# Optimization experiments

Hardware: AMD Instinct MI355X
Metric: run time of the kernel (lower is better)

Reference implementation:

```python
import jax, jax.numpy as jnp
import numpy as np

NUM_HEADS = 8
EPS = 1e-5  # torch GroupNorm default eps


def setup_inputs() -> dict:
    key = jax.random.key(0)
    ks = jax.random.split(key, 3)
    B, C, H, W = 8, 384, 32, 32
    x = jax.random.normal(ks[0], (B, C, H, W), dtype=jnp.float32)
    qkv_w = jax.random.normal(ks[1], (3 * C, C), dtype=jnp.float32) * 0.02
    proj_w = jax.random.normal(ks[2], (C, C), dtype=jnp.float32) * 0.02
    proj_b = jnp.zeros((C,), dtype=jnp.float32)
    lambda_param = jnp.ones((1, NUM_HEADS, 1, 1), dtype=jnp.float32) * 0.5
    gc = NUM_HEADS * ((C // NUM_HEADS) // 2)  # 192 group-norm channels
    gn_weight = jnp.ones((gc,), dtype=jnp.float32)
    gn_bias = jnp.zeros((gc,), dtype=jnp.float32)
    return {"x": x, "qkv_w": qkv_w, "lambda_param": lambda_param,
            "gn_weight": gn_weight, "gn_bias": gn_bias,
            "proj_w": proj_w, "proj_b": proj_b}


def reference(x, qkv_w, lambda_param, gn_weight, gn_bias, proj_w, proj_b):
    B, C, H, W = x.shape
    nh = NUM_HEADS
    hd = C // nh
    hd2 = hd // 2
    N = H * W
    scale = hd ** -0.5

    xf = x.reshape(B, C, N)
    qkv = jnp.einsum('oc,bcn->bon', qkv_w, xf)  # (B, 3C, N), 1x1 conv no bias
    q, k, v = jnp.split(qkv, 3, axis=1)
    q = q.reshape(B, nh, hd, N)
    k = k.reshape(B, nh, hd, N)
    v = v.reshape(B, nh, hd, N)

    q1, q2 = q[:, :, :hd2], q[:, :, hd2:]
    k1, k2 = k[:, :, :hd2], k[:, :, hd2:]
    v1, v2 = v[:, :, :hd2], v[:, :, hd2:]

    # GroupNorm(2 groups) on q2 viewed as (B, nh*hd2, H, W)
    gc = nh * hd2
    qg = q2.reshape(B, 2, (gc // 2) * N)  # normalize over (group channels, H, W)
    mean = qg.mean(axis=2, keepdims=True)
    var = qg.var(axis=2, keepdims=True)
    qg = (qg - mean) * jax.lax.rsqrt(var + EPS)
    q2n = qg.reshape(B, gc, N) * gn_weight[None, :, None] + gn_bias[None, :, None]
    q2n = q2n.reshape(B, nh, hd2, N)

    # dual softmax attention maps (B, nh, N, N)
    attn1 = jax.nn.softmax(jnp.einsum('bhdn,bhdm->bhnm', q1, k1) * scale, axis=-1)
    attn2 = jax.nn.softmax(jnp.einsum('bhdn,bhdm->bhnm', q2n, k2) * scale * lambda_param, axis=-1)
    diff = attn1 - attn2

    out1 = jnp.einsum('bhnm,bhdm->bhnd', diff, v1)  # (B, nh, N, hd2)
    out2 = jnp.einsum('bhnm,bhdm->bhnd', diff, v2)
    out = jnp.concatenate([out1, out2], axis=2)  # (B, nh, 2N, hd2) -- matches torch cat dim=2
    out = out.reshape(B, C, H, W)

    out = jnp.einsum('oc,bchw->bohw', proj_w, out) + proj_b[None, :, None, None]
    return out
```

## Files before the change

### kernel.cpp

```cpp
#include <hip/hip_runtime.h>
#include <hip/hip_bf16.h>
#include <stdint.h>

typedef _Float16 half8 __attribute__((ext_vector_type(8)));
typedef _Float16 half4 __attribute__((ext_vector_type(4)));
typedef __fp16 fp16x2 __attribute__((ext_vector_type(2)));
typedef float floatx4 __attribute__((ext_vector_type(4)));
typedef float floatx16 __attribute__((ext_vector_type(16)));

#define SCALE 0.14433756729740643f
#define LOG2E 1.4426950408889634f


__device__ inline float fexp2(float x) { return __builtin_exp2f(x); }

__device__ inline uint32_t pkrtz(float a, float b) {
  fp16x2 h = __builtin_amdgcn_cvt_pkrtz(a, b);
  union { fp16x2 h; uint32_t u; } cv; cv.h = h; return cv.u;
}

__launch_bounds__(256)
__global__ void k_prep(const float* __restrict__ qkv_w, const float* __restrict__ pw,
                       const float* __restrict__ x, _Float16* __restrict__ Wf,
                       _Float16* __restrict__ PWf, _Float16* __restrict__ Xt) {
  const int bid = blockIdx.x;
  if (bid < 288) {
    const float* src = (bid < 216) ? qkv_w : pw;
    _Float16* dst = (bid < 216) ? Wf : PWf;
    int cid = (bid < 216 ? bid : bid - 216) * 256 + threadIdx.x;
    int nchunks = (bid < 216) ? 55296 : 18432;
    if (cid >= nchunks) return;
    int lane = cid & 63;
    int t = cid >> 6;
    int cb = t % 12;
    int g16 = t / 12;
    const float* s = src + (long)(g16 * 16 + (lane & 15)) * 384 + cb * 32 + (lane >> 4) * 8;
    floatx4 a = *(const floatx4*)s;
    floatx4 b = *(const floatx4*)(s + 4);
    half8 h;
    #pragma unroll
    for (int j = 0; j < 4; j++) { h[j] = (_Float16)a[j]; h[j+4] = (_Float16)b[j]; }
    *(half8*)(dst + (long)cid * 8) = h;
  } else {
    int idx = bid - 288;
    const int cblk = idx % 12, nseg = (idx / 12) & 3, b = idx / 48;
    const float* S = x + ((long)b * 384 + cblk * 32) * 1024 + nseg * 256;
    _Float16* D = Xt + (long)b * 393216 + cblk * 32768 + (long)nseg * 256 * 32;
    __shared__ _Float16 T[32][264];
    const int wv = threadIdx.x >> 6, lane = threadIdx.x & 63;
    #pragma unroll
    for (int rr = 0; rr < 8; rr++) {
      int r = wv * 8 + rr;
      floatx4 v = *(const floatx4*)(S + (long)r * 1024 + lane * 4);
      half4 h;
      #pragma unroll
      for (int j = 0; j < 4; j++) h[j] = (_Float16)v[j];
      *(half4*)&T[r][lane * 4] = h;
    }
    __syncthreads();
    const int nn = threadIdx.x >> 3, c = (threadIdx.x & 7) * 4;
    #pragma unroll
    for (int p = 0; p < 8; p++) {
      int n = p * 32 + nn;
      half4 h;
      #pragma unroll
      for (int i = 0; i < 4; i++) h[i] = T[c + i][n];
      *(half4*)(D + (long)n * 32 + c) = h;
    }
  }
}

__launch_bounds__(256)
__global__ void k_trh(const _Float16* __restrict__ src, _Float16* __restrict__ dst) {
  const int cblk = blockIdx.x, nseg = blockIdx.y, b = blockIdx.z;
  const _Float16* S = src + ((long)b * 384 + cblk * 32) * 1024 + nseg * 256;
  _Float16* D = dst + (long)b * 393216 + cblk * 32768 + (long)nseg * 256 * 32;
  __shared__ _Float16 T[32][264];
  const int wv = threadIdx.x >> 6, lane = threadIdx.x & 63;
  #pragma unroll
  for (int rr = 0; rr < 8; rr++) {
    int r = wv * 8 + rr;
    *(half4*)&T[r][lane * 4] = *(const half4*)(S + (long)r * 1024 + lane * 4);
  }
  __syncthreads();
  const int nn = threadIdx.x >> 3, c = (threadIdx.x & 7) * 4;
  #pragma unroll
  for (int p = 0; p < 8; p++) {
    int n = p * 32 + nn;
    half4 h;
    #pragma unroll
    for (int i = 0; i < 4; i++) h[i] = T[c + i][n];
    *(half4*)(D + (long)n * 32 + c) = h;
  }
}

__launch_bounds__(256, 4)
__global__ void k_qkv(const _Float16* __restrict__ Xt, const _Float16* __restrict__ Wf,
                      _Float16* __restrict__ Qs, _Float16* __restrict__ Ks,
                      _Float16* __restrict__ Vs, float* __restrict__ gnpart) {
  const int tid = threadIdx.x;
  const int lane = tid & 63;
  const int wv = tid >> 6;
  const int l15 = lane & 15;
  const int g = lane >> 4;
  const int o0 = blockIdx.x * 48;
  const int n0 = blockIdx.y * 64;
  const int b = blockIdx.z;

  const int ncol = n0 + wv * 16 + l15;
  const _Float16* xp = Xt + (long)b * 393216 + (long)ncol * 32 + g * 8;
  const _Float16* wfb = Wf + (long)(blockIdx.x * 36) * 512 + lane * 8;

  half8 xb[12];
  #pragma unroll
  for (int cb = 0; cb < 12; cb++) xb[cb] = *(const half8*)(xp + cb * 32768);

  floatx4 zero4 = {0.f, 0.f, 0.f, 0.f};
  floatx4 acc0 = zero4, acc1 = zero4, acc2 = zero4;

  half8 A0 = *(const half8*)(wfb);
  half8 A1 = *(const half8*)(wfb + 12 * 512);
  half8 A2 = *(const half8*)(wfb + 24 * 512);
  #pragma unroll
  for (int cb = 0; cb < 12; cb++) {
    half8 c0 = A0, c1 = A1, c2 = A2;
    if (cb < 11) {
      A0 = *(const half8*)(wfb + (cb + 1) * 512);
      A1 = *(const half8*)(wfb + (12 + cb + 1) * 512);
      A2 = *(const half8*)(wfb + (24 + cb + 1) * 512);
    }
    acc0 = __builtin_amdgcn_mfma_f32_16x16x32_f16(c0, xb[cb], acc0, 0, 0, 0);
    acc1 = __builtin_amdgcn_mfma_f32_16x16x32_f16(c1, xb[cb], acc1, 0, 0, 0);
    acc2 = __builtin_amdgcn_mfma_f32_16x16x32_f16(c2, xb[cb], acc2, 0, 0, 0);
  }

  floatx4 acc[3] = {acc0, acc1, acc2};
  __shared__ __align__(16) _Float16 T[3456];
  __shared__ float red[8];

  if (o0 < 768) {
    #pragma unroll
    for (int rt = 0; rt < 3; rt++)
      #pragma unroll
      for (int r = 0; r < 4; r++)
        T[(wv * 16 + l15) * 52 + rt * 16 + g * 4 + r] = (_Float16)acc[rt][r];
    __syncthreads();
    const int qk = o0 >= 384;
    const int hh = (o0 - qk * 384) / 48;
    _Float16* base = (qk ? Ks : Qs) + (long)(b * 8 + hh) * 65536;
    #pragma unroll
    for (int it = 0; it < 2; it++) {
      int slot = it * 256 + tid;
      int ntl = slot >> 8;
      int t   = (slot >> 6) & 3;
      int ln  = slot & 63;
      int hi_s = ln >> 5, l31_s = ln & 31;
      int n_ = ntl * 32 + l31_s;
      int c0 = t * 16 + hi_s * 8;
      half8 val;
      #pragma unroll
      for (int j = 0; j < 8; j++) {
        int col = c0 + j;
        int d48 = col < 24 ? col : col - 8;
        bool isq = (col < 24) || (col >= 32 && col < 56);
        val[j] = isq ? T[n_ * 52 + d48] : (_Float16)0;
      }
      *(half8*)(base + ((((n0 >> 5) + ntl) * 4 + t) * 64 + ln) * 8) = val;
    }
    if (!qk) {
      float s1 = 0.f, s2 = 0.f;
      int n_ = tid >> 2, k0 = (tid & 3) * 6;
      #pragma unroll
      for (int k = 0; k < 6; k++) {
        float v = (float)T[n_ * 52 + 24 + k0 + k];
        s1 += v; s2 += v * v;
      }
      #pragma unroll
      for (int off = 32; off > 0; off >>= 1) {
        s1 += __shfl_down(s1, off);
        s2 += __shfl_down(s2, off);
      }
      if ((tid & 63) == 0) { red[tid >> 6] = s1; red[4 + (tid >> 6)] = s2; }
      __syncthreads();
      if (tid == 0) {
        int slot = (b * 8 + hh) * 16 + (n0 >> 6);
        gnpart[slot * 2]     = red[0] + red[1] + red[2] + red[3];
        gnpart[slot * 2 + 1] = red[4] + red[5] + red[6] + red[7];
      }
    }
  } else {
    #pragma unroll
    for (int rt = 0; rt < 3; rt++)
      #pragma unroll
      for (int r = 0; r < 4; r++)
        T[(rt * 16 + g * 4 + r) * 72 + wv * 16 + l15] = (_Float16)acc[rt][r];
    __syncthreads();
    const int hh = (o0 - 768) / 48;
    _Float16* base = Vs + (long)(b * 8 + hh) * 65536;
    #pragma unroll
    for (int it = 0; it < 2; it++) {
      int slot = it * 256 + tid;
      int lwin = slot >> 8;
      int ckc  = (slot >> 6) & 3;
      int kc   = ckc & 1, c = ckc >> 1;
      int ln = slot & 63;
      int hi_s = ln >> 5, l31_s = ln & 31;
      int d48 = c * 32 + l31_s;
      half8 val;
      if (d48 < 48) {
        int mb = lwin * 32 + kc * 16 + hi_s * 4;
        half4 a = *(const half4*)&T[d48 * 72 + mb];
        half4 bq = *(const half4*)&T[d48 * 72 + mb + 8];
        val[0] = a[0]; val[1] = a[1]; val[2] = a[2]; val[3] = a[3];
        val[4] = bq[0]; val[5] = bq[1]; val[6] = bq[2]; val[7] = bq[3];
      } else {
        _Float16 f = (d48 == 48) ? (_Float16)1 : (_Float16)0;
        #pragma unroll
        for (int j = 0; j < 8; j++) val[j] = f;
      }
      *(half8*)(base + ((((n0 >> 5) + lwin) * 4 + ckc) * 64 + ln) * 8) = val;
    }
  }
}

__launch_bounds__(512, 4)
__global__ void k_attn(const _Float16* __restrict__ Qs, const _Float16* __restrict__ Ks,
                       const _Float16* __restrict__ Vs, const float* __restrict__ gnpart,
                       const float* __restrict__ lam, const float* __restrict__ gw,
                       const float* __restrict__ gb, _Float16* __restrict__ Yf) {
  const int tid = threadIdx.x;
  const int lane = tid & 63;
  const int wv = tid >> 6;
  const int l31 = lane & 31;
  const int hi = lane >> 5;
  const int id = blockIdx.x;
  const int bh = ((id >> 6) << 3) | (id & 7);
  const int ntlgrp = (id >> 3) & 7;
  const int br = wv & 1;
  const int ntile = ntlgrp * 4 + (wv >> 1);
  const int n0 = ntile * 32;
  const int b = bh >> 3, h = bh & 7;

  const _Float16* Qp = Qs + (long)bh * 65536 + (ntile * 256 + lane) * 8;
  half8 qra = *(const half8*)(Qp + (2 * br) * 512);
  half8 qrb = *(const half8*)(Qp + (2 * br + 1) * 512);
  half8 qfa, qfb;
  if (br == 0) {
    const float s1s = SCALE * LOG2E;
    #pragma unroll
    for (int j = 0; j < 8; j++) {
      qfa[j] = (_Float16)((float)qra[j] * s1s);
      qfb[j] = (_Float16)((float)qrb[j] * s1s);
    }
  } else {
    const int grp = h >> 2;
    const float* pp = gnpart + (b * 128 + grp * 64) * 2;
    float S1 = pp[lane * 2], S2 = pp[lane * 2 + 1];
    #pragma unroll
    for (int off = 1; off < 64; off <<= 1) {
      S1 += __shfl_xor(S1, off);
      S2 += __shfl_xor(S2, off);
    }
    float mean = S1 * (1.f / 98304.f);
    float rstd = rsqrtf(S2 * (1.f / 98304.f) - mean * mean + 1e-5f);
    float sl = SCALE * LOG2E * lam[h];
    const float* gwp = gw + h * 24;
    const float* gbp = gb + h * 24;
    #pragma unroll
    for (int j = 0; j < 8; j++) {
      qfa[j] = (_Float16)((((float)qra[j] - mean) * rstd * gwp[hi * 8 + j] + gbp[hi * 8 + j]) * sl);
      qfb[j] = (_Float16)((((float)qrb[j] - mean) * rstd * gwp[16 + j] + gbp[16 + j]) * sl);
    }
  }

  const _Float16* gK = Ks + (long)bh * 65536 + ((wv >> 2) * 2048 + (wv & 3) * 512) + lane * 8;
  const _Float16* gV = Vs + (long)bh * 65536 + ((wv >> 2) * 2048 + (wv & 3) * 512) + lane * 8;

  __shared__ __align__(16) char smem[32768];
  const int ldsK = wv * 1024 + lane * 16;
  const int ldsV = 8192 + wv * 1024 + lane * 16;

  floatx16 z16;
  #pragma unroll
  for (int i = 0; i < 16; i++) z16[i] = 0.f;
  floatx16 accA = z16, accB = z16;

  {
    uint4 a = *(const uint4*)gK;
    uint4 c = *(const uint4*)gV;
    *(uint4*)(smem + ldsK) = a;
    *(uint4*)(smem + ldsV) = c;
  }
  __syncthreads();

  #pragma unroll 2
  for (int i = 0; i < 16; i++) {
    const int cur = (i & 1) << 14;
    uint4 sa, sc;
    if (i < 15) {
      sa = *(const uint4*)(gK + (i + 1) * 4096);
      sc = *(const uint4*)(gV + (i + 1) * 4096);
    }
    #pragma unroll
    for (int j = 0; j < 2; j++) {
      const char* Kb = smem + cur + j * 4096;
      const char* Vb = smem + cur + 8192 + j * 4096;
      half8 kfa = *(const half8*)(Kb + (2 * br) * 1024 + lane * 16);
      half8 kfb = *(const half8*)(Kb + (2 * br + 1) * 1024 + lane * 16);

      floatx16 s = __builtin_amdgcn_mfma_f32_32x32x16_f16(kfa, qfa, z16, 0, 0, 0);
      s = __builtin_amdgcn_mfma_f32_32x32x16_f16(kfb, qfb, s, 0, 0, 0);

      half8 vf0 = *(const half8*)(Vb + lane * 16);
      half8 vf1 = *(const half8*)(Vb + 1024 + lane * 16);
      half8 vf2 = *(const half8*)(Vb + 2048 + lane * 16);
      half8 vf3 = *(const half8*)(Vb + 3072 + lane * 16);

      uint32_t u[8];
      #pragma unroll
      for (int q = 0; q < 8; q++)
        u[q] = pkrtz(fexp2(s[2 * q]), fexp2(s[2 * q + 1]));

      union { uint32_t u[4]; half8 h; } pa;
      pa.u[0] = u[0]; pa.u[1] = u[1]; pa.u[2] = u[2]; pa.u[3] = u[3];
      half8 pc0 = pa.h;
      pa.u[0] = u[4]; pa.u[1] = u[5]; pa.u[2] = u[6]; pa.u[3] = u[7];
      half8 pc1 = pa.h;

      accA = __builtin_amdgcn_mfma_f32_32x32x16_f16(pc0, vf0, accA, 0, 0, 0);
      accA = __builtin_amdgcn_mfma_f32_32x32x16_f16(pc1, vf1, accA, 0, 0, 0);
      accB = __builtin_amdgcn_mfma_f32_32x32x16_f16(pc0, vf2, accB, 0, 0, 0);
      accB = __builtin_amdgcn_mfma_f32_32x32x16_f16(pc1, vf3, accB, 0, 0, 0);
    }
    if (i < 15) {
      *(uint4*)(smem + (cur ^ 16384) + ldsK) = sa;
      *(uint4*)(smem + (cur ^ 16384) + ldsV) = sc;
    }
    __syncthreads();
  }

  const int pairid = wv >> 1;
  float* rbuf = (float*)(smem + pairid * 8192);
  if (br == 1) {
    #pragma unroll
    for (int r = 0; r < 16; r++) {
      rbuf[r * 64 + lane] = accA[r];
      rbuf[(16 + r) * 64 + lane] = accB[r];
    }
  }
  __syncthreads();
  if (br == 0) {
    float a2a[16], a2b[16];
    #pragma unroll
    for (int r = 0; r < 16; r++) {
      a2a[r] = rbuf[r * 64 + lane];
      a2b[r] = rbuf[(16 + r) * 64 + lane];
    }
    _Float16* Ybh = Yf + (long)bh * 49152;
    const int src = (lane & 32) + 16;
    #pragma unroll
    for (int r = 0; r < 16; r++) {
      float i1 = __builtin_amdgcn_rcpf(__shfl(accB[r], src));
      float i2 = __builtin_amdgcn_rcpf(__shfl(a2b[r], src));
      int n = n0 + (r & 3) + 8 * ((r >> 2) & 3) + 4 * hi;
      float o0 = accA[r] * i1 - a2a[r] * i2;
      float o1 = accB[r] * i1 - a2b[r] * i2;
      int p0 = l31 >= 24;
      Ybh[p0 * 24576 + n * 24 + (l31 - p0 * 24)] = (_Float16)o0;
      if (l31 < 16) Ybh[24576 + n * 24 + 8 + l31] = (_Float16)o1;
    }
  }
}

__launch_bounds__(256, 4)
__global__ void k_proj(const _Float16* __restrict__ Yt, const _Float16* __restrict__ PWf,
                       const float* __restrict__ PB, float* __restrict__ out) {
  const int tid = threadIdx.x, lane = tid & 63, wv = tid >> 6, l15 = lane & 15, g = lane >> 4;
  const int o0 = blockIdx.x * 64, m0 = blockIdx.y * 64, b = blockIdx.z;

  const int mcol = m0 + wv * 16 + l15;
  const _Float16* yp = Yt + (long)b * 393216 + (long)mcol * 32 + g * 8;
  const _Float16* wfb = PWf + (long)(blockIdx.x * 48) * 512 + lane * 8;

  half8 yb[12];
  #pragma unroll
  for (int cb = 0; cb < 12; cb++) yb[cb] = *(const half8*)(yp + cb * 32768);

  floatx4 zero4 = {0.f, 0.f, 0.f, 0.f};
  floatx4 acc0 = zero4, acc1 = zero4, acc2 = zero4, acc3 = zero4;

  half8 A0 = *(const half8*)(wfb);
  half8 A1 = *(const half8*)(wfb + 12 * 512);
  half8 A2 = *(const half8*)(wfb + 24 * 512);
  half8 A3 = *(const half8*)(wfb + 36 * 512);
  #pragma unroll
  for (int cb = 0; cb < 12; cb++) {
    half8 c0 = A0, c1 = A1, c2 = A2, c3 = A3;
    if (cb < 11) {
      A0 = *(const half8*)(wfb + (cb + 1) * 512);
      A1 = *(const half8*)(wfb + (12 + cb + 1) * 512);
      A2 = *(const half8*)(wfb + (24 + cb + 1) * 512);
      A3 = *(const half8*)(wfb + (36 + cb + 1) * 512);
    }
    acc0 = __builtin_amdgcn_mfma_f32_16x16x32_f16(c0, yb[cb], acc0, 0, 0, 0);
    acc1 = __builtin_amdgcn_mfma_f32_16x16x32_f16(c1, yb[cb], acc1, 0, 0, 0);
    acc2 = __builtin_amdgcn_mfma_f32_16x16x32_f16(c2, yb[cb], acc2, 0, 0, 0);
    acc3 = __builtin_amdgcn_mfma_f32_16x16x32_f16(c3, yb[cb], acc3, 0, 0, 0);
  }

  floatx4 acc[4] = {acc0, acc1, acc2, acc3};
  #pragma unroll
  for (int rt = 0; rt < 4; rt++) {
    int o_ = o0 + rt * 16 + g * 4;
    #pragma unroll
    for (int r = 0; r < 4; r++) {
      out[(long)(b * 384 + o_ + r) * 1024 + mcol] = acc[rt][r] + PB[o_ + r];
    }
  }
}

extern "C" void kernel_launch(void* const* d_in, const int* in_sizes, int n_in,
                              void* d_out, int out_size, void* d_ws, size_t ws_size,
                              hipStream_t stream) {
  const float* x     = (const float*)d_in[0];
  const float* qkv_w = (const float*)d_in[1];
  const float* lam   = (const float*)d_in[2];
  const float* gw    = (const float*)d_in[3];
  const float* gb    = (const float*)d_in[4];
  const float* pw    = (const float*)d_in[5];
  const float* pb    = (const float*)d_in[6];
  float* out = (float*)d_out;
  char* ws = (char*)d_ws;
  _Float16* Qs  = (_Float16*)ws;
  _Float16* Ks  = (_Float16*)(ws + 8388608);
  _Float16* Vs  = (_Float16*)(ws + 16777216);
  float* gnpart   = (float*)(ws + 25165824);
  _Float16* Yf  = (_Float16*)(ws + 26214400);
  _Float16* Xt  = (_Float16*)(ws + 37752832);
  _Float16* Yt  = (_Float16*)(ws + 44044288);
  _Float16* Wf  = (_Float16*)(ws + 50335744);
  _Float16* PWf = (_Float16*)(ws + 51220480);

  hipLaunchKernelGGL(k_prep,    dim3(672),        dim3(256), 0, stream, qkv_w, pw, x, Wf, PWf, Xt);
  hipLaunchKernelGGL(k_qkv,     dim3(24, 16, 8),  dim3(256), 0, stream, Xt, Wf, Qs, Ks, Vs, gnpart);
  hipLaunchKernelGGL(k_attn,    dim3(512),        dim3(512), 0, stream, Qs, Ks, Vs, gnpart, lam, gw, gb, Yf);
  hipLaunchKernelGGL(k_trh,     dim3(12, 4, 8),   dim3(256), 0, stream, Yf, Yt);
  hipLaunchKernelGGL(k_proj,    dim3(6, 16, 8),   dim3(256), 0, stream, Yt, PWf, pb, out);
}
```

Baseline: 93.26 us.

## Stage weights in LDS for GEMMs; deepen attention K/V prefetch with rotated start

The qkv and proj GEMM kernels now load their per-block weight tiles cooperatively into shared memory once, with each wave loading a slice, instead of every wave streaming the full weight tile from global memory. The qkv kernel reuses that buffer as its transpose scratch after a barrier. The attention kernel moves from a two-stage to a four-stage LDS ring, keeping K/V loads two iterations ahead in registers. It also rotates the starting KV tile per block to spread memory traffic, and raises wave priority around the MFMA section. The larger 64KB LDS footprint may lower how many attention blocks fit per CU, and the extra barriers add sync cost in the GEMMs.

After: 84.33 us. 9.6% less time.

```diff
diff --git a/kernel.cpp b/kernel.cpp
--- a/kernel.cpp
+++ b/kernel.cpp
@@ -107,36 +107,42 @@
   const int n0 = blockIdx.y * 64;
   const int b = blockIdx.z;
 
+  __shared__ __align__(16) _Float16 WA[18432];
+  __shared__ float red[8];
+
+  {
+    const _Float16* wsrc = Wf + ((long)blockIdx.x * 36 + wv * 9) * 512 + lane * 8;
+    uint4 wtmp[9];
+    #pragma unroll
+    for (int k = 0; k < 9; k++) wtmp[k] = *(const uint4*)(wsrc + k * 512);
+    #pragma unroll
+    for (int k = 0; k < 9; k++) *(uint4*)(&WA[(wv * 9 + k) * 512 + lane * 8]) = wtmp[k];
+  }
+
   const int ncol = n0 + wv * 16 + l15;
   const _Float16* xp = Xt + (long)b * 393216 + (long)ncol * 32 + g * 8;
-  const _Float16* wfb = Wf + (long)(blockIdx.x * 36) * 512 + lane * 8;
-
   half8 xb[12];
   #pragma unroll
   for (int cb = 0; cb < 12; cb++) xb[cb] = *(const half8*)(xp + cb * 32768);
+
+  __syncthreads();
 
   floatx4 zero4 = {0.f, 0.f, 0.f, 0.f};
   floatx4 acc0 = zero4, acc1 = zero4, acc2 = zero4;
 
-  half8 A0 = *(const half8*)(wfb);
-  half8 A1 = *(const half8*)(wfb + 12 * 512);
-  half8 A2 = *(const half8*)(wfb + 24 * 512);
   #pragma unroll
   for (int cb = 0; cb < 12; cb++) {
-    half8 c0 = A0, c1 = A1, c2 = A2;
-    if (cb < 11) {
-      A0 = *(const half8*)(wfb + (cb + 1) * 512);
-      A1 = *(const half8*)(wfb + (12 + cb + 1) * 512);
-      A2 = *(const half8*)(wfb + (24 + cb + 1) * 512);
-    }
-    acc0 = __builtin_amdgcn_mfma_f32_16x16x32_f16(c0, xb[cb], acc0, 0, 0, 0);
-    acc1 = __builtin_amdgcn_mfma_f32_16x16x32_f16(c1, xb[cb], acc1, 0, 0, 0);
-    acc2 = __builtin_amdgcn_mfma_f32_16x16x32_f16(c2, xb[cb], acc2, 0, 0, 0);
+    half8 a0 = *(const half8*)&WA[(cb) * 512 + lane * 8];
+    half8 a1 = *(const half8*)&WA[(12 + cb) * 512 + lane * 8];
+    half8 a2 = *(const half8*)&WA[(24 + cb) * 512 + lane * 8];
+    acc0 = __builtin_amdgcn_mfma_f32_16x16x32_f16(a0, xb[cb], acc0, 0, 0, 0);
+    acc1 = __builtin_amdgcn_mfma_f32_16x16x32_f16(a1, xb[cb], acc1, 0, 0, 0);
+    acc2 = __builtin_amdgcn_mfma_f32_16x16x32_f16(a2, xb[cb], acc2, 0, 0, 0);
   }
 
   floatx4 acc[3] = {acc0, acc1, acc2};
-  __shared__ __align__(16) _Float16 T[3456];
-  __shared__ float red[8];
+  __syncthreads();
+  _Float16* T = WA;
 
   if (o0 < 768) {
     #pragma unroll
@@ -240,6 +246,7 @@
   const int ntile = ntlgrp * 4 + (wv >> 1);
   const int n0 = ntile * 32;
   const int b = bh >> 3, h = bh & 7;
+  const int rot = ((id >> 3) & 7) << 1;
 
   const _Float16* Qp = Qs + (long)bh * 65536 + (ntile * 256 + lane) * 8;
   half8 qra = *(const half8*)(Qp + (2 * br) * 512);
@@ -276,7 +283,7 @@
   const _Float16* gK = Ks + (long)bh * 65536 + ((wv >> 2) * 2048 + (wv & 3) * 512) + lane * 8;
   const _Float16* gV = Vs + (long)bh * 65536 + ((wv >> 2) * 2048 + (wv & 3) * 512) + lane * 8;
 
-  __shared__ __align__(16) char smem[32768];
+  __shared__ __align__(16) char smem[65536];
   const int ldsK = wv * 1024 + lane * 16;
   const int ldsV = 8192 + wv * 1024 + lane * 16;
 
@@ -285,22 +292,31 @@
   for (int i = 0; i < 16; i++) z16[i] = 0.f;
   floatx16 accA = z16, accB = z16;
 
+  uint4 ka, va, kb2, vb2, kc, vc;
   {
-    uint4 a = *(const uint4*)gK;
-    uint4 c = *(const uint4*)gV;
-    *(uint4*)(smem + ldsK) = a;
-    *(uint4*)(smem + ldsV) = c;
-  }
-  __syncthreads();
-
-  #pragma unroll 2
+    uint4 k0 = *(const uint4*)(gK + (long)(((0 + rot) & 15) * 4096));
+    uint4 v0 = *(const uint4*)(gV + (long)(((0 + rot) & 15) * 4096));
+    uint4 k1 = *(const uint4*)(gK + (long)(((1 + rot) & 15) * 4096));
+    uint4 v1 = *(const uint4*)(gV + (long)(((1 + rot) & 15) * 4096));
+    ka  = *(const uint4*)(gK + (long)(((2 + rot) & 15) * 4096));
+    va  = *(const uint4*)(gV + (long)(((2 + rot) & 15) * 4096));
+    kb2 = *(const uint4*)(gK + (long)(((3 + rot) & 15) * 4096));
+    vb2 = *(const uint4*)(gV + (long)(((3 + rot) & 15) * 4096));
+    *(uint4*)(smem + ldsK) = k0;
+    *(uint4*)(smem + ldsV) = v0;
+    *(uint4*)(smem + 16384 + ldsK) = k1;
+    *(uint4*)(smem + 16384 + ldsV) = v1;
+  }
+  __syncthreads();
+
+  #pragma unroll
   for (int i = 0; i < 16; i++) {
-    const int cur = (i & 1) << 14;
-    uint4 sa, sc;
-    if (i < 15) {
-      sa = *(const uint4*)(gK + (i + 1) * 4096);
-      sc = *(const uint4*)(gV + (i + 1) * 4096);
-    }
+    if (i + 4 < 16) {
+      kc = *(const uint4*)(gK + (long)(((i + 4 + rot) & 15) * 4096));
+      vc = *(const uint4*)(gV + (long)(((i + 4 + rot) & 15) * 4096));
+    }
+    const int cur = (i & 3) << 14;
+    __builtin_amdgcn_s_setprio(1);
     #pragma unroll
     for (int j = 0; j < 2; j++) {
       const char* Kb = smem + cur + j * 4096;
@@ -332,10 +348,13 @@
       accB = __builtin_amdgcn_mfma_f32_32x32x16_f16(pc0, vf2, accB, 0, 0, 0);
       accB = __builtin_amdgcn_mfma_f32_32x32x16_f16(pc1, vf3, accB, 0, 0, 0);
     }
-    if (i < 15) {
-      *(uint4*)(smem + (cur ^ 16384) + ldsK) = sa;
-      *(uint4*)(smem + (cur ^ 16384) + ldsV) = sc;
-    }
+    __builtin_amdgcn_s_setprio(0);
+    if (i + 2 < 16) {
+      const int wb = ((i + 2) & 3) << 14;
+      *(uint4*)(smem + wb + ldsK) = ka;
+      *(uint4*)(smem + wb + ldsV) = va;
+    }
+    ka = kb2; va = vb2; kb2 = kc; vb2 = vc;
     __syncthreads();
   }
 
@@ -378,34 +397,38 @@
   const int tid = threadIdx.x, lane = tid & 63, wv = tid >> 6, l15 = lane & 15, g = lane >> 4;
   const int o0 = blockIdx.x * 64, m0 = blockIdx.y * 64, b = blockIdx.z;
 
+  __shared__ __align__(16) _Float16 PA[24576];
+
+  {
+    const _Float16* psrc = PWf + ((long)blockIdx.x * 48 + wv * 12) * 512 + lane * 8;
+    uint4 ptmp[12];
+    #pragma unroll
+    for (int k = 0; k < 12; k++) ptmp[k] = *(const uint4*)(psrc + k * 512);
+    #pragma unroll
+    for (int k = 0; k < 12; k++) *(uint4*)(&PA[(wv * 12 + k) * 512 + lane * 8]) = ptmp[k];
+  }
+
   const int mcol = m0 + wv * 16 + l15;
   const _Float16* yp = Yt + (long)b * 393216 + (long)mcol * 32 + g * 8;
-  const _Float16* wfb = PWf + (long)(blockIdx.x * 48) * 512 + lane * 8;
-
   half8 yb[12];
   #pragma unroll
   for (int cb = 0; cb < 12; cb++) yb[cb] = *(const half8*)(yp + cb * 32768);
+
+  __syncthreads();
 
   floatx4 zero4 = {0.f, 0.f, 0.f, 0.f};
   floatx4 acc0 = zero4, acc1 = zero4, acc2 = zero4, acc3 = zero4;
 
-  half8 A0 = *(const half8*)(wfb);
-  half8 A1 = *(const half8*)(wfb + 12 * 512);
-  half8 A2 = *(const half8*)(wfb + 24 * 512);
-  half8 A3 = *(const half8*)(wfb + 36 * 512);
   #pragma unroll
   for (int cb = 0; cb < 12; cb++) {
-    half8 c0 = A0, c1 = A1, c2 = A2, c3 = A3;
-    if (cb < 11) {
-      A0 = *(const half8*)(wfb + (cb + 1) * 512);
-      A1 = *(const half8*)(wfb + (12 + cb + 1) * 512);
-      A2 = *(const half8*)(wfb + (24 + cb + 1) * 512);
-      A3 = *(const half8*)(wfb + (36 + cb + 1) * 512);
-    }
-    acc0 = __builtin_amdgcn_mfma_f32_16x16x32_f16(c0, yb[cb], acc0, 0, 0, 0);
-    acc1 = __builtin_amdgcn_mfma_f32_16x16x32_f16(c1, yb[cb], acc1, 0, 0, 0);
-    acc2 = __builtin_amdgcn_mfma_f32_16x16x32_f16(c2, yb[cb], acc2, 0, 0, 0);
-    acc3 = __builtin_amdgcn_mfma_f32_16x16x32_f16(c3, yb[cb], acc3, 0, 0, 0);
+    half8 a0 = *(const half8*)&PA[(cb) * 512 + lane * 8];
+    half8 a1 = *(const half8*)&PA[(12 + cb) * 512 + lane * 8];
+    half8 a2 = *(const half8*)&PA[(24 + cb) * 512 + lane * 8];
+    half8 a3 = *(const half8*)&PA[(36 + cb) * 512 + lane * 8];
+    acc0 = __builtin_amdgcn_mfma_f32_16x16x32_f16(a0, yb[cb], acc0, 0, 0, 0);
+    acc1 = __builtin_amdgcn_mfma_f32_16x16x32_f16(a1, yb[cb], acc1, 0, 0, 0);
+    acc2 = __builtin_amdgcn_mfma_f32_16x16x32_f16(a2, yb[cb], acc2, 0, 0, 0);
+    acc3 = __builtin_amdgcn_mfma_f32_16x16x32_f16(a3, yb[cb], acc3, 0, 0, 0);
   }
 
   floatx4 acc[4] = {acc0, acc1, acc2, acc3};
```
